# Kernel tuning notes

Measured on AMD Instinct MI355X. Metric: run time of the kernel, lower is better.

The kernel has to match this reference:

```python
import jax, jax.numpy as jnp
import numpy as np

HIDDEN = 1024
N_HEADS = 16
HEAD_DIM = HIDDEN // N_HEADS
WINDOW = 256  # symmetric window: keys j with i - W//2 <= j <= i + W//2
BATCH, SEQ = 2, 2048


def setup_inputs() -> dict:
    key = jax.random.key(0)
    ks = jax.random.split(key, 9)
    s = 0.02
    return {
        "x":  jax.random.normal(ks[0], (BATCH, SEQ, HIDDEN), dtype=jnp.float32),
        "wq": jax.random.normal(ks[1], (HIDDEN, HIDDEN), dtype=jnp.float32) * s,
        "bq": jnp.zeros((HIDDEN,), dtype=jnp.float32),
        "wk": jax.random.normal(ks[2], (HIDDEN, HIDDEN), dtype=jnp.float32) * s,
        "bk": jnp.zeros((HIDDEN,), dtype=jnp.float32),
        "wv": jax.random.normal(ks[3], (HIDDEN, HIDDEN), dtype=jnp.float32) * s,
        "bv": jnp.zeros((HIDDEN,), dtype=jnp.float32),
        "wo": jax.random.normal(ks[4], (HIDDEN, HIDDEN), dtype=jnp.float32) * s,
        "bo": jnp.zeros((HIDDEN,), dtype=jnp.float32),
    }


def reference(x, wq, bq, wk, bk, wv, bv, wo, bo):
    B, S, Hs = x.shape
    scale = HEAD_DIM ** -0.5

    def proj(w, b):
        # [B,S,Hs] -> [B,H,S,D]
        return (x @ w + b).reshape(B, S, N_HEADS, HEAD_DIM).transpose(0, 2, 1, 3)

    q = proj(wq, bq)
    k = proj(wk, bk)
    v = proj(wv, bv)

    # Clipped sliding window == band-masked full attention (identical softmax weights).
    scores = jnp.einsum('bhid,bhjd->bhij', q, k) * scale  # [B,H,S,S]
    i = jnp.arange(S)[:, None]
    j = jnp.arange(S)[None, :]
    band = (j >= i - WINDOW // 2) & (j <= i + WINDOW // 2)
    scores = jnp.where(band, scores, -jnp.inf)
    attn = jax.nn.softmax(scores, axis=-1)
    out = jnp.einsum('bhij,bhjd->bhid', attn, v)  # [B,H,S,D]
    out = out.transpose(0, 2, 1, 3).reshape(B, S, Hs)
    return out @ wo + bo
```

## Files before the change

### kernel.cpp

```cpp
#include <hip/hip_runtime.h>
#include <hip/hip_bf16.h>
#include <stdint.h>

#define BATCH 2
#define SEQ   2048
#define HID   1024
#define NH    16
#define HD    64
#define W2    128

using bhalf8 = __attribute__((ext_vector_type(8))) short;
using fvec4  = __attribute__((ext_vector_type(4))) float;
using u16x8  = __attribute__((ext_vector_type(8))) unsigned short;

__device__ __forceinline__ unsigned short f2bf(float f) {
    union { float f; unsigned int u; } c; c.f = f;
    unsigned int u = c.u;
    u += 0x7FFFu + ((u >> 16) & 1u);
    return (unsigned short)(u >> 16);
}

__device__ __forceinline__ fvec4 zero4() {
    fvec4 z = {0.f, 0.f, 0.f, 0.f};
    return z;
}

__device__ __forceinline__ void load_lds16(const void* g, void* l) {
    __builtin_amdgcn_global_load_lds(
        (const __attribute__((address_space(1))) void*)g,
        (__attribute__((address_space(3))) void*)l, 16, 0, 0);
}

__device__ __forceinline__ float rowmax16(float v) {
    v = fmaxf(v, __shfl_xor(v, 1));
    v = fmaxf(v, __shfl_xor(v, 2));
    v = fmaxf(v, __shfl_xor(v, 4));
    v = fmaxf(v, __shfl_xor(v, 8));
    return v;
}
__device__ __forceinline__ float rowsum16(float v) {
    v += __shfl_xor(v, 1);
    v += __shfl_xor(v, 2);
    v += __shfl_xor(v, 4);
    v += __shfl_xor(v, 8);
    return v;
}


__global__ __launch_bounds__(256) void k_convert_x(const float* __restrict__ x,
                                                   unsigned short* __restrict__ xb) {
    int i = (blockIdx.x * 256 + threadIdx.x) * 8;
    float4 a = *(const float4*)(x + i);
    float4 b = *(const float4*)(x + i + 4);
    u16x8 o;
    o[0] = f2bf(a.x); o[1] = f2bf(a.y); o[2] = f2bf(a.z); o[3] = f2bf(a.w);
    o[4] = f2bf(b.x); o[5] = f2bf(b.y); o[6] = f2bf(b.z); o[7] = f2bf(b.w);
    *(u16x8*)(xb + i) = o;
}

__global__ __launch_bounds__(256) void k_transpose_w(
    const float* __restrict__ w0, const float* __restrict__ w1,
    const float* __restrict__ w2, const float* __restrict__ w3,
    unsigned short* __restrict__ t0, unsigned short* __restrict__ t1,
    unsigned short* __restrict__ t2, unsigned short* __restrict__ t3) {
    int z = blockIdx.z;
    const float* src = (z == 0) ? w0 : (z == 1) ? w1 : (z == 2) ? w2 : w3;
    unsigned short* dst = (z == 0) ? t0 : (z == 1) ? t1 : (z == 2) ? t2 : t3;
    __shared__ float tile[32][33];
    int n0 = blockIdx.x * 32, k0 = blockIdx.y * 32;
    int tx = threadIdx.x, ty = threadIdx.y;
#pragma unroll
    for (int r = 0; r < 4; ++r)
        tile[ty + 8 * r][tx] = src[(size_t)(k0 + ty + 8 * r) * HID + n0 + tx];
    __syncthreads();
#pragma unroll
    for (int r = 0; r < 4; ++r)
        dst[(size_t)(n0 + ty + 8 * r) * HID + k0 + tx] = f2bf(tile[tx][ty + 8 * r]);
}


__device__ __forceinline__ void stage_tile(const unsigned short* __restrict__ A,
                                           const unsigned short* __restrict__ Bt,
                                           int m0, int n0, int k0,
                                           unsigned short* As, unsigned short* Bs,
                                           int t) {
#pragma unroll
    for (int i = 0; i < 2; ++i) {
        int slot = t + 256 * i;
        int row = slot >> 2, ch = slot & 3;
        int chs = ch ^ ((row >> 1) & 3);
        load_lds16(A + (size_t)(m0 + row) * HID + k0 + chs * 8, As + slot * 8);
        load_lds16(Bt + (size_t)(n0 + row) * HID + k0 + chs * 8, Bs + slot * 8);
    }
}

__device__ __forceinline__ void gemm_tile(const unsigned short* __restrict__ A,
                                          const unsigned short* __restrict__ Bt,
                                          int m0, int n0,
                                          unsigned short (*As)[128 * 32],
                                          unsigned short (*Bs)[128 * 32],
                                          fvec4 acc[4][4]) {
    const int t = threadIdx.x;
    const int lane = t & 63;
    const int wid = t >> 6;
    const int wr = wid >> 1, wc = wid & 1;
    const int c16 = lane & 15, g = lane >> 4;

#pragma unroll
    for (int mi = 0; mi < 4; ++mi)
#pragma unroll
        for (int ni = 0; ni < 4; ++ni) acc[mi][ni] = zero4();

    stage_tile(A, Bt, m0, n0, 0, As[0], Bs[0], t);
    stage_tile(A, Bt, m0, n0, 32, As[1], Bs[1], t);

    int cur = 0, sb = 2;
    for (int k0 = 0; k0 < HID; k0 += 32) {
        if (k0 + 32 < HID)
            asm volatile("s_waitcnt vmcnt(4)" ::: "memory");
        else
            asm volatile("s_waitcnt vmcnt(0)" ::: "memory");
        asm volatile("s_waitcnt lgkmcnt(0)" ::: "memory");
        __builtin_amdgcn_sched_barrier(0);
        __builtin_amdgcn_s_barrier();

        if (k0 + 64 < HID) {
            stage_tile(A, Bt, m0, n0, k0 + 64, As[sb], Bs[sb], t);
            sb = (sb == 2) ? 0 : sb + 1;
        }

        const unsigned short* Ab = As[cur];
        const unsigned short* Bb = Bs[cur];
        bhalf8 af[4], bf[4];
#pragma unroll
        for (int i = 0; i < 4; ++i) {
            int ra = wr * 64 + i * 16 + c16;
            int rb = wc * 64 + i * 16 + c16;
            af[i] = *(const bhalf8*)(Ab + ra * 32 + (g ^ ((ra >> 1) & 3)) * 8);
            bf[i] = *(const bhalf8*)(Bb + rb * 32 + (g ^ ((rb >> 1) & 3)) * 8);
        }
#pragma unroll
        for (int mi = 0; mi < 4; ++mi)
#pragma unroll
            for (int ni = 0; ni < 4; ++ni)
                acc[mi][ni] = __builtin_amdgcn_mfma_f32_16x16x32_bf16(
                    af[mi], bf[ni], acc[mi][ni], 0, 0, 0);
        cur = (cur == 2) ? 0 : cur + 1;
    }
}

__global__ __launch_bounds__(256) void k_gemm_qkv(
    const unsigned short* __restrict__ xb,
    const unsigned short* __restrict__ wqt, const unsigned short* __restrict__ wkt,
    const unsigned short* __restrict__ wvt,
    const float* __restrict__ bq, const float* __restrict__ bk, const float* __restrict__ bv,
    unsigned short* __restrict__ qb, unsigned short* __restrict__ kbuf,
    unsigned short* __restrict__ vt) {
    __shared__ unsigned short As[3][128 * 32];
    __shared__ unsigned short Bs[3][128 * 32];
    const int z = blockIdx.z;
    const unsigned short* Bt = (z == 0) ? wqt : (z == 1) ? wkt : wvt;
    const float* bias = (z == 0) ? bq : (z == 1) ? bk : bv;
    const int m0 = blockIdx.y * 128, n0 = blockIdx.x * 128;
    fvec4 acc[4][4];
    gemm_tile(xb, Bt, m0, n0, As, Bs, acc);

    const int lane = threadIdx.x & 63, wid = threadIdx.x >> 6;
    const int wr = wid >> 1, wc = wid & 1, c16 = lane & 15, g = lane >> 4;
#pragma unroll
    for (int mi = 0; mi < 4; ++mi) {
#pragma unroll
        for (int ni = 0; ni < 4; ++ni) {
            int gcol = n0 + wc * 64 + ni * 16 + c16;
            int h = gcol >> 6, d = gcol & 63;
            float bsv = bias[gcol];
#pragma unroll
            for (int r = 0; r < 4; ++r) {
                int grow = m0 + wr * 64 + mi * 16 + 4 * g + r;
                int b = grow >> 11, s = grow & (SEQ - 1);
                float v = acc[mi][ni][r] + bsv;
                if (z == 0)
                    qb[((size_t)(b * NH + h) * SEQ + s) * HD + d] = f2bf(v * 0.125f);
                else if (z == 1)
                    kbuf[((size_t)(b * NH + h) * SEQ + s) * HD + d] = f2bf(v);
                else
                    vt[((size_t)(b * NH + h) * HD + d) * SEQ + s] = f2bf(v);
            }
        }
    }
}

__global__ __launch_bounds__(256) void k_gemm_out(
    const unsigned short* __restrict__ attn, const unsigned short* __restrict__ wot,
    const float* __restrict__ bo, float* __restrict__ out) {
    __shared__ unsigned short As[3][128 * 32];
    __shared__ unsigned short Bs[3][128 * 32];
    const int m0 = blockIdx.y * 128, n0 = blockIdx.x * 128;
    fvec4 acc[4][4];
    gemm_tile(attn, wot, m0, n0, As, Bs, acc);

    const int lane = threadIdx.x & 63, wid = threadIdx.x >> 6;
    const int wr = wid >> 1, wc = wid & 1, c16 = lane & 15, g = lane >> 4;
#pragma unroll
    for (int mi = 0; mi < 4; ++mi) {
#pragma unroll
        for (int ni = 0; ni < 4; ++ni) {
            int gcol = n0 + wc * 64 + ni * 16 + c16;
            float bsv = bo[gcol];
#pragma unroll
            for (int r = 0; r < 4; ++r) {
                int grow = m0 + wr * 64 + mi * 16 + 4 * g + r;
                out[(size_t)grow * HID + gcol] = acc[mi][ni][r] + bsv;
            }
        }
    }
}

__global__ __launch_bounds__(256) void k_attn(
    const unsigned short* __restrict__ qb, const unsigned short* __restrict__ kbuf,
    const unsigned short* __restrict__ vt, unsigned short* __restrict__ attn) {
    const int bh = blockIdx.y;
    const int wid = threadIdx.x >> 6, lane = threadIdx.x & 63;
    const int g = lane >> 4, c16 = lane & 15;
    const int q0 = blockIdx.x * 64 + wid * 16;

    const unsigned short* Qp = qb + (size_t)bh * SEQ * HD;
    const unsigned short* Kp = kbuf + (size_t)bh * SEQ * HD;
    const unsigned short* Vp = vt + (size_t)bh * HD * SEQ;

    __shared__ unsigned short Plds[4][16 * 32];
    unsigned short* myP = Plds[wid];

    bhalf8 qf0, qf1;
    {
        const unsigned short* p = Qp + (size_t)(q0 + c16) * HD + g * 8;
        qf0 = *(const bhalf8*)p;
        qf1 = *(const bhalf8*)(p + 32);
    }
    fvec4 acc[4];
#pragma unroll
    for (int i = 0; i < 4; ++i) acc[i] = zero4();
    float mrow[4] = {-1e30f, -1e30f, -1e30f, -1e30f};
    float srow[4] = {0.f, 0.f, 0.f, 0.f};

    int kstart = q0 - W2; if (kstart < 0) kstart = 0; kstart &= ~31;
    int kend = q0 + 15 + W2; if (kend > SEQ - 1) kend = SEQ - 1;

    for (int t0 = kstart; t0 <= kend; t0 += 32) {
        fvec4 sc0 = zero4(), sc1 = zero4();
        {
            const unsigned short* kp = Kp + (size_t)(t0 + c16) * HD + g * 8;
            bhalf8 ka = *(const bhalf8*)kp;
            bhalf8 kb2 = *(const bhalf8*)(kp + 32);
            sc0 = __builtin_amdgcn_mfma_f32_16x16x32_bf16(qf0, ka, sc0, 0, 0, 0);
            sc0 = __builtin_amdgcn_mfma_f32_16x16x32_bf16(qf1, kb2, sc0, 0, 0, 0);
        }
        {
            const unsigned short* kp = Kp + (size_t)(t0 + 16 + c16) * HD + g * 8;
            bhalf8 ka = *(const bhalf8*)kp;
            bhalf8 kb2 = *(const bhalf8*)(kp + 32);
            sc1 = __builtin_amdgcn_mfma_f32_16x16x32_bf16(qf0, ka, sc1, 0, 0, 0);
            sc1 = __builtin_amdgcn_mfma_f32_16x16x32_bf16(qf1, kb2, sc1, 0, 0, 0);
        }
#pragma unroll
        for (int r = 0; r < 4; ++r) {
            int ia = q0 + 4 * g + r;
            int j0 = t0 + c16, j1 = t0 + 16 + c16;
            if (j0 < ia - W2 || j0 > ia + W2) sc0[r] = -1e30f;
            if (j1 < ia - W2 || j1 > ia + W2) sc1[r] = -1e30f;
        }
#pragma unroll
        for (int r = 0; r < 4; ++r) {
            float pm = rowmax16(fmaxf(sc0[r], sc1[r]));
            float mn = fmaxf(mrow[r], pm);
            float f = __expf(mrow[r] - mn);
            mrow[r] = mn;
            float p0 = __expf(sc0[r] - mn);
            float p1 = __expf(sc1[r] - mn);
            srow[r] = srow[r] * f + (p0 + p1);
#pragma unroll
            for (int db = 0; db < 4; ++db) acc[db][r] *= f;
            myP[(4 * g + r) * 32 + c16] = f2bf(p0);
            myP[(4 * g + r) * 32 + 16 + c16] = f2bf(p1);
        }
        asm volatile("s_waitcnt lgkmcnt(0)" ::: "memory");
        __builtin_amdgcn_sched_barrier(0);
        bhalf8 pf = *(const bhalf8*)(myP + c16 * 32 + g * 8);
#pragma unroll
        for (int db = 0; db < 4; ++db) {
            const unsigned short* vp = Vp + (size_t)(db * 16 + c16) * SEQ + t0 + g * 8;
            bhalf8 vf = *(const bhalf8*)vp;
            acc[db] = __builtin_amdgcn_mfma_f32_16x16x32_bf16(pf, vf, acc[db], 0, 0, 0);
        }
    }

    float inv[4];
#pragma unroll
    for (int r = 0; r < 4; ++r) inv[r] = 1.f / rowsum16(srow[r]);

    const int b = bh >> 4, h = bh & 15;
#pragma unroll
    for (int db = 0; db < 4; ++db)
#pragma unroll
        for (int r = 0; r < 4; ++r) {
            int si = q0 + 4 * g + r;
            attn[((size_t)(b * SEQ) + si) * HID + h * HD + db * 16 + c16] =
                f2bf(acc[db][r] * inv[r]);
        }
}


extern "C" void kernel_launch(void* const* d_in, const int* in_sizes, int n_in,
                              void* d_out, int out_size, void* d_ws, size_t ws_size,
                              hipStream_t stream) {
    const float* x  = (const float*)d_in[0];
    const float* wq = (const float*)d_in[1];
    const float* bq = (const float*)d_in[2];
    const float* wk = (const float*)d_in[3];
    const float* bk = (const float*)d_in[4];
    const float* wv = (const float*)d_in[5];
    const float* bv = (const float*)d_in[6];
    const float* wo = (const float*)d_in[7];
    const float* bo = (const float*)d_in[8];
    float* out = (float*)d_out;

    char* ws = (char*)d_ws;
    unsigned short* xb   = (unsigned short*)(ws);
    unsigned short* wqt  = (unsigned short*)(ws + (8u << 20));
    unsigned short* wkt  = wqt + 1024 * 1024;
    unsigned short* wvt  = wkt + 1024 * 1024;
    unsigned short* wot  = wvt + 1024 * 1024;
    unsigned short* qb   = wot + 1024 * 1024;
    unsigned short* kbuf = qb + 4u * 1024 * 1024;
    unsigned short* vt   = kbuf + 4u * 1024 * 1024;
    unsigned short* attn = vt + 4u * 1024 * 1024;

    k_convert_x<<<dim3(2048), dim3(256), 0, stream>>>(x, xb);
    k_transpose_w<<<dim3(32, 32, 4), dim3(32, 8), 0, stream>>>(wq, wk, wv, wo,
                                                               wqt, wkt, wvt, wot);
    k_gemm_qkv<<<dim3(8, 32, 3), dim3(256), 0, stream>>>(xb, wqt, wkt, wvt,
                                                         bq, bk, bv, qb, kbuf, vt);
    k_attn<<<dim3(SEQ / 64, BATCH * NH), dim3(256), 0, stream>>>(qb, kbuf, vt, attn);
    k_gemm_out<<<dim3(8, 32), dim3(256), 0, stream>>>(attn, wot, bo, out);
}
```

Baseline: 189.4 us.

## Use 8-wave GEMM blocks and LDS-staged coalesced V-transpose store

Both GEMM kernels move from 4 waves to 8 waves per 128x128 tile, with each wave computing a 64x32 sub-tile. Each thread now stages one 16-byte chunk per operand per k-step, and the vmcnt waits are adjusted to match. The V projection epilogue writes the tile transposed into LDS and then stores vt with 16-byte coalesced row writes instead of scattered 2-byte strided stores. This aims for more latency hiding and better store efficiency, at the cost of more B-fragment reloads per wave and an extra LDS round trip with barriers.

```diff
diff --git a/kernel.cpp b/kernel.cpp
--- a/kernel.cpp
+++ b/kernel.cpp
@@ -84,40 +84,35 @@
                                            int m0, int n0, int k0,
                                            unsigned short* As, unsigned short* Bs,
                                            int t) {
-#pragma unroll
-    for (int i = 0; i < 2; ++i) {
-        int slot = t + 256 * i;
-        int row = slot >> 2, ch = slot & 3;
-        int chs = ch ^ ((row >> 1) & 3);
-        load_lds16(A + (size_t)(m0 + row) * HID + k0 + chs * 8, As + slot * 8);
-        load_lds16(Bt + (size_t)(n0 + row) * HID + k0 + chs * 8, Bs + slot * 8);
-    }
-}
-
-__device__ __forceinline__ void gemm_tile(const unsigned short* __restrict__ A,
-                                          const unsigned short* __restrict__ Bt,
-                                          int m0, int n0,
-                                          unsigned short (*As)[128 * 32],
-                                          unsigned short (*Bs)[128 * 32],
-                                          fvec4 acc[4][4]) {
+    int row = t >> 2, ch = t & 3;
+    int chs = ch ^ ((row >> 1) & 3);
+    load_lds16(A + (size_t)(m0 + row) * HID + k0 + chs * 8, As + t * 8);
+    load_lds16(Bt + (size_t)(n0 + row) * HID + k0 + chs * 8, Bs + t * 8);
+}
+
+__device__ __forceinline__ void gemm_tile8(const unsigned short* __restrict__ A,
+                                           const unsigned short* __restrict__ Bt,
+                                           int m0, int n0,
+                                           unsigned short* As, unsigned short* Bs,
+                                           fvec4 acc[4][2]) {
     const int t = threadIdx.x;
     const int lane = t & 63;
     const int wid = t >> 6;
-    const int wr = wid >> 1, wc = wid & 1;
+    const int wr = wid >> 2, wc = wid & 3;
     const int c16 = lane & 15, g = lane >> 4;
 
 #pragma unroll
     for (int mi = 0; mi < 4; ++mi)
 #pragma unroll
-        for (int ni = 0; ni < 4; ++ni) acc[mi][ni] = zero4();
-
-    stage_tile(A, Bt, m0, n0, 0, As[0], Bs[0], t);
-    stage_tile(A, Bt, m0, n0, 32, As[1], Bs[1], t);
+        for (int ni = 0; ni < 2; ++ni) acc[mi][ni] = zero4();
+
+    stage_tile(A, Bt, m0, n0, 0, As, Bs, t);
+    stage_tile(A, Bt, m0, n0, 32, As + 4096, Bs + 4096, t);
 
     int cur = 0, sb = 2;
     for (int k0 = 0; k0 < HID; k0 += 32) {
         if (k0 + 32 < HID)
-            asm volatile("s_waitcnt vmcnt(4)" ::: "memory");
+            asm volatile("s_waitcnt vmcnt(2)" ::: "memory");
         else
             asm volatile("s_waitcnt vmcnt(0)" ::: "memory");
         asm volatile("s_waitcnt lgkmcnt(0)" ::: "memory");
@@ -125,87 +120,115 @@
         __builtin_amdgcn_s_barrier();
 
         if (k0 + 64 < HID) {
-            stage_tile(A, Bt, m0, n0, k0 + 64, As[sb], Bs[sb], t);
+            stage_tile(A, Bt, m0, n0, k0 + 64, As + sb * 4096, Bs + sb * 4096, t);
             sb = (sb == 2) ? 0 : sb + 1;
         }
 
-        const unsigned short* Ab = As[cur];
-        const unsigned short* Bb = Bs[cur];
-        bhalf8 af[4], bf[4];
+        const unsigned short* Ab = As + cur * 4096;
+        const unsigned short* Bb = Bs + cur * 4096;
+        bhalf8 af[4], bf[2];
 #pragma unroll
         for (int i = 0; i < 4; ++i) {
             int ra = wr * 64 + i * 16 + c16;
-            int rb = wc * 64 + i * 16 + c16;
             af[i] = *(const bhalf8*)(Ab + ra * 32 + (g ^ ((ra >> 1) & 3)) * 8);
+        }
+#pragma unroll
+        for (int i = 0; i < 2; ++i) {
+            int rb = wc * 32 + i * 16 + c16;
             bf[i] = *(const bhalf8*)(Bb + rb * 32 + (g ^ ((rb >> 1) & 3)) * 8);
         }
 #pragma unroll
         for (int mi = 0; mi < 4; ++mi)
 #pragma unroll
-            for (int ni = 0; ni < 4; ++ni)
+            for (int ni = 0; ni < 2; ++ni)
                 acc[mi][ni] = __builtin_amdgcn_mfma_f32_16x16x32_bf16(
                     af[mi], bf[ni], acc[mi][ni], 0, 0, 0);
         cur = (cur == 2) ? 0 : cur + 1;
     }
 }
 
-__global__ __launch_bounds__(256) void k_gemm_qkv(
+__global__ __launch_bounds__(512, 6) void k_gemm_qkv(
     const unsigned short* __restrict__ xb,
     const unsigned short* __restrict__ wqt, const unsigned short* __restrict__ wkt,
     const unsigned short* __restrict__ wvt,
     const float* __restrict__ bq, const float* __restrict__ bk, const float* __restrict__ bv,
     unsigned short* __restrict__ qb, unsigned short* __restrict__ kbuf,
     unsigned short* __restrict__ vt) {
-    __shared__ unsigned short As[3][128 * 32];
-    __shared__ unsigned short Bs[3][128 * 32];
+    __shared__ unsigned short SH[2][3 * 128 * 32];
     const int z = blockIdx.z;
     const unsigned short* Bt = (z == 0) ? wqt : (z == 1) ? wkt : wvt;
     const float* bias = (z == 0) ? bq : (z == 1) ? bk : bv;
     const int m0 = blockIdx.y * 128, n0 = blockIdx.x * 128;
-    fvec4 acc[4][4];
-    gemm_tile(xb, Bt, m0, n0, As, Bs, acc);
-
-    const int lane = threadIdx.x & 63, wid = threadIdx.x >> 6;
-    const int wr = wid >> 1, wc = wid & 1, c16 = lane & 15, g = lane >> 4;
-#pragma unroll
-    for (int mi = 0; mi < 4; ++mi) {
-#pragma unroll
-        for (int ni = 0; ni < 4; ++ni) {
-            int gcol = n0 + wc * 64 + ni * 16 + c16;
+    fvec4 acc[4][2];
+    gemm_tile8(xb, Bt, m0, n0, SH[0], SH[1], acc);
+
+    const int t = threadIdx.x, lane = t & 63, wid = t >> 6;
+    const int wr = wid >> 2, wc = wid & 3, c16 = lane & 15, g = lane >> 4;
+
+    if (z != 2) {
+#pragma unroll
+        for (int mi = 0; mi < 4; ++mi) {
+#pragma unroll
+            for (int ni = 0; ni < 2; ++ni) {
+                int gcol = n0 + wc * 32 + ni * 16 + c16;
+                int h = gcol >> 6, d = gcol & 63;
+                float bsv = bias[gcol];
+#pragma unroll
+                for (int r = 0; r < 4; ++r) {
+                    int grow = m0 + wr * 64 + mi * 16 + 4 * g + r;
+                    int b = grow >> 11, s = grow & (SEQ - 1);
+                    float v = acc[mi][ni][r] + bsv;
+                    if (z == 0)
+                        qb[((size_t)(b * NH + h) * SEQ + s) * HD + d] = f2bf(v * 0.125f);
+                    else
+                        kbuf[((size_t)(b * NH + h) * SEQ + s) * HD + d] = f2bf(v);
+                }
+            }
+        }
+    } else {
+        unsigned short* VL = &SH[0][0];
+        __syncthreads();
+#pragma unroll
+        for (int mi = 0; mi < 4; ++mi)
+#pragma unroll
+            for (int ni = 0; ni < 2; ++ni) {
+                int dl = wc * 32 + ni * 16 + c16;
+                float bsv = bias[n0 + dl];
+#pragma unroll
+                for (int r = 0; r < 4; ++r) {
+                    int sl = wr * 64 + mi * 16 + 4 * g + r;
+                    VL[dl * 132 + sl] = f2bf(acc[mi][ni][r] + bsv);
+                }
+            }
+        __syncthreads();
+        const int b = m0 >> 11, sbase = m0 & (SEQ - 1);
+#pragma unroll
+        for (int it = 0; it < 4; ++it) {
+            int slot = t + 512 * it;
+            int dl = slot >> 4, ch = slot & 15;
+            int gcol = n0 + dl;
             int h = gcol >> 6, d = gcol & 63;
-            float bsv = bias[gcol];
-#pragma unroll
-            for (int r = 0; r < 4; ++r) {
-                int grow = m0 + wr * 64 + mi * 16 + 4 * g + r;
-                int b = grow >> 11, s = grow & (SEQ - 1);
-                float v = acc[mi][ni][r] + bsv;
-                if (z == 0)
-                    qb[((size_t)(b * NH + h) * SEQ + s) * HD + d] = f2bf(v * 0.125f);
-                else if (z == 1)
-                    kbuf[((size_t)(b * NH + h) * SEQ + s) * HD + d] = f2bf(v);
-                else
-                    vt[((size_t)(b * NH + h) * HD + d) * SEQ + s] = f2bf(v);
-            }
-        }
-    }
-}
-
-__global__ __launch_bounds__(256) void k_gemm_out(
+            u16x8 v = *(const u16x8*)(VL + dl * 132 + ch * 8);
+            *(u16x8*)(vt + ((size_t)(b * NH + h) * HD + d) * SEQ + sbase + ch * 8) = v;
+        }
+    }
+}
+
+__global__ __launch_bounds__(512, 6) void k_gemm_out(
     const unsigned short* __restrict__ attn, const unsigned short* __restrict__ wot,
     const float* __restrict__ bo, float* __restrict__ out) {
-    __shared__ unsigned short As[3][128 * 32];
-    __shared__ unsigned short Bs[3][128 * 32];
+    __shared__ unsigned short SH[2][3 * 128 * 32];
     const int m0 = blockIdx.y * 128, n0 = blockIdx.x * 128;
-    fvec4 acc[4][4];
-    gemm_tile(attn, wot, m0, n0, As, Bs, acc);
+    fvec4 acc[4][2];
+    gemm_tile8(attn, wot, m0, n0, SH[0], SH[1], acc);
 
     const int lane = threadIdx.x & 63, wid = threadIdx.x >> 6;
-    const int wr = wid >> 1, wc = wid & 1, c16 = lane & 15, g = lane >> 4;
+    const int wr = wid >> 2, wc = wid & 3, c16 = lane & 15, g = lane >> 4;
 #pragma unroll
     for (int mi = 0; mi < 4; ++mi) {
 #pragma unroll
-        for (int ni = 0; ni < 4; ++ni) {
-            int gcol = n0 + wc * 64 + ni * 16 + c16;
+        for (int ni = 0; ni < 2; ++ni) {
+            int gcol = n0 + wc * 32 + ni * 16 + c16;
             float bsv = bo[gcol];
 #pragma unroll
             for (int r = 0; r < 4; ++r) {
@@ -338,8 +361,8 @@
     k_convert_x<<<dim3(2048), dim3(256), 0, stream>>>(x, xb);
     k_transpose_w<<<dim3(32, 32, 4), dim3(32, 8), 0, stream>>>(wq, wk, wv, wo,
                                                                wqt, wkt, wvt, wot);
-    k_gemm_qkv<<<dim3(8, 32, 3), dim3(256), 0, stream>>>(xb, wqt, wkt, wvt,
+    k_gemm_qkv<<<dim3(8, 32, 3), dim3(512), 0, stream>>>(xb, wqt, wkt, wvt,
                                                          bq, bk, bv, qb, kbuf, vt);
     k_attn<<<dim3(SEQ / 64, BATCH * NH), dim3(256), 0, stream>>>(qb, kbuf, vt, attn);
-    k_gemm_out<<<dim3(8, 32), dim3(256), 0, stream>>>(attn, wot, bo, out);
-}
+    k_gemm_out<<<dim3(8, 32), dim3(512), 0, stream>>>(attn, wot, bo, out);
+}
```

After: 181.2 us. -4.3%, faster.
